# Kernel tuning notes

Hardware: AMD Instinct MI355X
Metric: run time of the kernel (lower is better)

Reference implementation:

```python
import jax, jax.numpy as jnp
import numpy as np

N_NODES = 50000
N_EDGES = 800000
D = 128
L = 3


def setup_inputs() -> dict:
    key = jax.random.key(0)
    k1, k2, k3 = jax.random.split(key, 3)
    x = jax.random.normal(k1, (N_NODES, D), dtype=jnp.float32)
    edge_index = jax.random.randint(k2, (2, N_EDGES), 0, N_NODES, dtype=jnp.int64)
    # per-layer GCNConv weights [L, in, out], bias [L, out] (zeros, as nn.Linear default bias is small),
    # PReLU per-channel slopes initialized to 0.25 (torch default)
    Ws = jax.random.normal(k3, (L, D, D), dtype=jnp.float32) / np.sqrt(D)
    bs = jnp.zeros((L, D), dtype=jnp.float32)
    alphas = jnp.full((L, D), 0.25, dtype=jnp.float32)
    return {"x": x, "edge_index": edge_index, "Ws": Ws, "bs": bs, "alphas": alphas}


def reference(x, edge_index, Ws, bs, alphas):
    N = x.shape[0]
    # PyG gcn_norm with edge_weight=None: unit weights, add self-loops (fill value 1),
    # symmetric normalization deg^{-1/2}[row] * deg^{-1/2}[col], aggregate at col (target).
    loop = jnp.arange(N, dtype=edge_index.dtype)
    row = jnp.concatenate([edge_index[0], loop])  # [E+N] source
    col = jnp.concatenate([edge_index[1], loop])  # [E+N] target
    deg = jax.ops.segment_sum(jnp.ones(row.shape[0], x.dtype), col, num_segments=N)
    dinv = jax.lax.rsqrt(deg)  # deg >= 1 due to self-loops
    norm = dinv[row] * dinv[col]  # [E+N]

    z = x
    for l in range(Ws.shape[0]):
        h = z @ Ws[l]  # linear transform [N, D]
        # gather -> scale -> scatter-add aggregation
        agg = jax.ops.segment_sum(h[row] * norm[:, None], col, num_segments=N)
        out = agg + bs[l]
        z = jnp.where(out >= 0, out, alphas[l] * out)  # per-channel PReLU
    return z
```

## Files before the change

### kernel.cpp

```cpp
#include <hip/hip_runtime.h>

#define N_NODES 50000
#define N_EDGES 800000
#define D 128
#define L 3
#define SCAN_B 1024
#define SCAN_NB ((N_NODES + SCAN_B - 1) / SCAN_B)


__global__ __launch_bounds__(256) void deg_init_k(unsigned int* deg) {
  int i = blockIdx.x * 256 + threadIdx.x;
  if (i < N_NODES) deg[i] = 1u;
}

__global__ __launch_bounds__(256) void deg_count_k(const int* __restrict__ col,
                                                   unsigned int* deg,
                                                   unsigned int* __restrict__ rank) {
  int e = blockIdx.x * 256 + threadIdx.x;
  if (e < N_EDGES) rank[e] = atomicAdd(&deg[col[e]], 1u);
}

__global__ __launch_bounds__(256) void dinv_k(float* dinv_f, const unsigned int* deg) {
  int i = blockIdx.x * 256 + threadIdx.x;
  if (i < N_NODES) dinv_f[i] = rsqrtf((float)deg[i]);
}

__global__ __launch_bounds__(SCAN_B) void scan1_k(const unsigned int* __restrict__ deg,
                                                  unsigned int* __restrict__ rowptr,
                                                  unsigned int* __restrict__ bsum) {
  __shared__ unsigned int buf[SCAN_B];
  const int tid = threadIdx.x;
  const int i = blockIdx.x * SCAN_B + tid;
  unsigned int d = (i < N_NODES) ? (deg[i] - 1u) : 0u;
  buf[tid] = d;
  __syncthreads();
  for (int off = 1; off < SCAN_B; off <<= 1) {
    unsigned int t = (tid >= off) ? buf[tid - off] : 0u;
    __syncthreads();
    buf[tid] += t;
    __syncthreads();
  }
  if (i < N_NODES) rowptr[i] = buf[tid] - d;
  if (tid == SCAN_B - 1) bsum[blockIdx.x] = buf[tid];
}

__global__ __launch_bounds__(64) void scan2_k(const unsigned int* __restrict__ bsum,
                                              unsigned int* __restrict__ boff,
                                              unsigned int* __restrict__ rowptr) {
  int lane = threadIdx.x;
  unsigned int v = (lane < SCAN_NB) ? bsum[lane] : 0u;
  unsigned int incl = v;
#pragma unroll
  for (int off = 1; off < 64; off <<= 1) {
    unsigned int t = __shfl_up(incl, off, 64);
    if (lane >= off) incl += t;
  }
  if (lane < SCAN_NB) boff[lane] = incl - v;
  if (lane == 63) rowptr[N_NODES] = incl;
}

__global__ __launch_bounds__(SCAN_B) void scan3_k(const unsigned int* __restrict__ boff,
                                                  unsigned int* __restrict__ rowptr) {
  int i = blockIdx.x * SCAN_B + threadIdx.x;
  if (i < N_NODES) rowptr[i] += boff[blockIdx.x];
}

__global__ __launch_bounds__(256) void fill_k(const int* __restrict__ rows,
                                              const int* __restrict__ cols,
                                              const unsigned int* __restrict__ rowptr,
                                              const unsigned int* __restrict__ rank,
                                              unsigned int* __restrict__ csr) {
  int e = blockIdx.x * 256 + threadIdx.x;
  if (e >= N_EDGES) return;
  csr[rowptr[cols[e]] + rank[e] - 1u] = (unsigned int)rows[e];
}

__global__ __launch_bounds__(256) void gather_k(const unsigned int* __restrict__ rowptr,
                                                const unsigned int* __restrict__ csr,
                                                const float* __restrict__ dinv,
                                                const float* __restrict__ Z,
                                                float* __restrict__ AGG) {
  int wid = (blockIdx.x * 256 + threadIdx.x) >> 6;
  int lane = threadIdx.x & 63;
  if (wid >= N_NODES) return;
  const float2* Z2 = (const float2*)Z;
  float di = dinv[wid];
  float2 z = Z2[(size_t)wid * 64 + lane];
  float sx = di * z.x, sy = di * z.y;
  unsigned int p = rowptr[wid], p1 = rowptr[wid + 1];
  for (; p + 4 <= p1; p += 4) {
    unsigned int s0 = csr[p], s1 = csr[p + 1], s2 = csr[p + 2], s3 = csr[p + 3];
    float w0 = dinv[s0], w1 = dinv[s1], w2 = dinv[s2], w3 = dinv[s3];
    float2 v0 = Z2[(size_t)s0 * 64 + lane];
    float2 v1 = Z2[(size_t)s1 * 64 + lane];
    float2 v2 = Z2[(size_t)s2 * 64 + lane];
    float2 v3 = Z2[(size_t)s3 * 64 + lane];
    sx += w0 * v0.x + w1 * v1.x + w2 * v2.x + w3 * v3.x;
    sy += w0 * v0.y + w1 * v1.y + w2 * v2.y + w3 * v3.y;
  }
  for (; p < p1; ++p) {
    unsigned int s0 = csr[p];
    float w0 = dinv[s0];
    float2 v0 = Z2[(size_t)s0 * 64 + lane];
    sx += w0 * v0.x;
    sy += w0 * v0.y;
  }
  float2 r;
  r.x = sx * di;
  r.y = sy * di;
  ((float2*)AGG)[(size_t)wid * 64 + lane] = r;
}

__global__ __launch_bounds__(256) void gemm_k(const float* __restrict__ P,
                                              const float* __restrict__ W,
                                              const float* __restrict__ bias,
                                              const float* __restrict__ alpha,
                                              float* __restrict__ out) {
  __shared__ float sW[32 * 128];
  __shared__ float sZ[128 * 33];
  const int tid = threadIdx.x;
  const int rb = blockIdx.x * 128;
  const int rg = tid >> 4, cg = tid & 15;
  const int r0 = rg * 8, c0 = cg * 8;
  float acc[8][8];
#pragma unroll
  for (int i = 0; i < 8; ++i)
#pragma unroll
    for (int j = 0; j < 8; ++j) acc[i][j] = 0.f;

  for (int kc = 0; kc < 128; kc += 32) {
    const float4* Wg = (const float4*)(W + (size_t)kc * 128);
#pragma unroll
    for (int i = 0; i < 4; ++i)
      ((float4*)sW)[tid + i * 256] = Wg[tid + i * 256];
#pragma unroll
    for (int i = 0; i < 4; ++i) {
      int idx = tid + i * 256;
      int r = idx >> 3, k4 = idx & 7;
      int gr = rb + r;
      float4 v = make_float4(0.f, 0.f, 0.f, 0.f);
      if (gr < N_NODES) v = *(const float4*)(P + (size_t)gr * D + kc + k4 * 4);
      float* dst = &sZ[r * 33 + k4 * 4];
      dst[0] = v.x; dst[1] = v.y; dst[2] = v.z; dst[3] = v.w;
    }
    __syncthreads();
#pragma unroll 8
    for (int k = 0; k < 32; ++k) {
      float zz[8], ww[8];
#pragma unroll
      for (int i = 0; i < 8; ++i) zz[i] = sZ[(r0 + i) * 33 + k];
      float4 wa = *(const float4*)&sW[k * 128 + c0];
      float4 wb = *(const float4*)&sW[k * 128 + c0 + 4];
      ww[0] = wa.x; ww[1] = wa.y; ww[2] = wa.z; ww[3] = wa.w;
      ww[4] = wb.x; ww[5] = wb.y; ww[6] = wb.z; ww[7] = wb.w;
#pragma unroll
      for (int i = 0; i < 8; ++i)
#pragma unroll
        for (int j = 0; j < 8; ++j) acc[i][j] = fmaf(zz[i], ww[j], acc[i][j]);
    }
    __syncthreads();
  }

  float bl[8], al[8];
#pragma unroll
  for (int j = 0; j < 8; ++j) {
    bl[j] = bias[c0 + j];
    al[j] = alpha[c0 + j];
  }
#pragma unroll
  for (int i = 0; i < 8; ++i) {
    int gr = rb + r0 + i;
    if (gr >= N_NODES) continue;
    float o[8];
#pragma unroll
    for (int j = 0; j < 8; ++j) {
      float v = acc[i][j] + bl[j];
      o[j] = v >= 0.f ? v : al[j] * v;
    }
    float4* dst = (float4*)(out + (size_t)gr * D + c0);
    dst[0] = make_float4(o[0], o[1], o[2], o[3]);
    dst[1] = make_float4(o[4], o[5], o[6], o[7]);
  }
}


extern "C" void kernel_launch(void* const* d_in, const int* in_sizes, int n_in,
                              void* d_out, int out_size, void* d_ws, size_t ws_size,
                              hipStream_t stream) {
  const float* x      = (const float*)d_in[0];
  const int*   ei     = (const int*)d_in[1];
  const float* Ws     = (const float*)d_in[2];
  const float* bs     = (const float*)d_in[3];
  const float* alphas = (const float*)d_in[4];
  float* out = (float*)d_out;

  const int* rows = ei;
  const int* cols = ei + N_EDGES;

  char* ws = (char*)d_ws;
  const size_t NPAD = (((size_t)N_NODES * 4 + 255) / 256) * 256;
  const size_t NP1PAD = ((((size_t)N_NODES + 1) * 4 + 255) / 256) * 256;
  float*        dinv   = (float*)ws;             ws += NPAD;
  unsigned int* rowptr = (unsigned int*)ws;      ws += NP1PAD;
  unsigned int* deg    = (unsigned int*)ws;      ws += NPAD;
  unsigned int* bsum   = (unsigned int*)ws;      ws += 256;
  unsigned int* boff   = (unsigned int*)ws;      ws += 256;
  unsigned int* csr    = (unsigned int*)ws;      ws += (size_t)N_EDGES * 4;
  float*        AGG    = (float*)ws;
  unsigned int* rank = (unsigned int*)AGG;
  float* Z = out;

  deg_init_k<<<(N_NODES + 255) / 256, 256, 0, stream>>>(deg);
  deg_count_k<<<(N_EDGES + 255) / 256, 256, 0, stream>>>(cols, deg, rank);
  dinv_k<<<(N_NODES + 255) / 256, 256, 0, stream>>>(dinv, deg);
  scan1_k<<<SCAN_NB, SCAN_B, 0, stream>>>(deg, rowptr, bsum);
  scan2_k<<<1, 64, 0, stream>>>(bsum, boff, rowptr);
  scan3_k<<<SCAN_NB, SCAN_B, 0, stream>>>(boff, rowptr);
  fill_k<<<(N_EDGES + 255) / 256, 256, 0, stream>>>(rows, cols, rowptr, rank, csr);

  for (int l = 0; l < L; ++l) {
    const float* zin = (l == 0) ? x : Z;
    gather_k<<<(N_NODES * 64 + 255) / 256, 256, 0, stream>>>(rowptr, csr, dinv, zin, AGG);
    gemm_k<<<(N_NODES + 127) / 128, 256, 0, stream>>>(
        AGG, Ws + (size_t)l * D * D, bs + (size_t)l * D, alphas + (size_t)l * D, Z);
  }
}
```

Baseline: 342.4 us.

## Cooperative wave-wide neighbor index loads in gather; transpose GEMM LDS tile for vector reads

In the aggregation kernel, each wave now loads up to 64 neighbor indices and their dinv weights in one coalesced read and broadcasts them with shuffles. It then issues 8 independent row loads at a time, replacing per-lane redundant scalar index and weight loads and raising memory-level parallelism. In the GEMM, the activation tile in shared memory is stored transposed with padding so the inner loop reads 8 rows with two float4 LDS loads instead of 8 scalar loads. The cost is strided scalar writes into LDS during tile fill and extra shuffle instructions in the gather.

Result: no change. 338.2 us (-1.2%).

```diff
diff --git a/kernel.cpp b/kernel.cpp
--- a/kernel.cpp
+++ b/kernel.cpp
@@ -87,23 +87,41 @@
   float di = dinv[wid];
   float2 z = Z2[(size_t)wid * 64 + lane];
   float sx = di * z.x, sy = di * z.y;
-  unsigned int p = rowptr[wid], p1 = rowptr[wid + 1];
-  for (; p + 4 <= p1; p += 4) {
-    unsigned int s0 = csr[p], s1 = csr[p + 1], s2 = csr[p + 2], s3 = csr[p + 3];
-    float w0 = dinv[s0], w1 = dinv[s1], w2 = dinv[s2], w3 = dinv[s3];
-    float2 v0 = Z2[(size_t)s0 * 64 + lane];
-    float2 v1 = Z2[(size_t)s1 * 64 + lane];
-    float2 v2 = Z2[(size_t)s2 * 64 + lane];
-    float2 v3 = Z2[(size_t)s3 * 64 + lane];
-    sx += w0 * v0.x + w1 * v1.x + w2 * v2.x + w3 * v3.x;
-    sy += w0 * v0.y + w1 * v1.y + w2 * v2.y + w3 * v3.y;
-  }
-  for (; p < p1; ++p) {
-    unsigned int s0 = csr[p];
-    float w0 = dinv[s0];
-    float2 v0 = Z2[(size_t)s0 * 64 + lane];
-    sx += w0 * v0.x;
-    sy += w0 * v0.y;
+  unsigned int p0 = rowptr[wid], p1 = rowptr[wid + 1];
+  for (unsigned int base = p0; base < p1; base += 64u) {
+    unsigned int cnt = p1 - base;
+    if (cnt > 64u) cnt = 64u;
+    unsigned int s = 0u;
+    float w = 0.f;
+    if (lane < (int)cnt) {
+      s = csr[base + lane];
+      w = dinv[s];
+    }
+    unsigned int j = 0;
+    for (; j + 8u <= cnt; j += 8u) {
+      unsigned int ss[8];
+      float wws[8];
+#pragma unroll
+      for (int t = 0; t < 8; ++t) {
+        ss[t] = __shfl(s, (int)(j + t), 64);
+        wws[t] = __shfl(w, (int)(j + t), 64);
+      }
+      float2 v[8];
+#pragma unroll
+      for (int t = 0; t < 8; ++t) v[t] = Z2[(size_t)ss[t] * 64 + lane];
+#pragma unroll
+      for (int t = 0; t < 8; ++t) {
+        sx += wws[t] * v[t].x;
+        sy += wws[t] * v[t].y;
+      }
+    }
+    for (; j < cnt; ++j) {
+      unsigned int s0 = __shfl(s, (int)j, 64);
+      float w0 = __shfl(w, (int)j, 64);
+      float2 v0 = Z2[(size_t)s0 * 64 + lane];
+      sx += w0 * v0.x;
+      sy += w0 * v0.y;
+    }
   }
   float2 r;
   r.x = sx * di;
@@ -117,7 +135,7 @@
                                               const float* __restrict__ alpha,
                                               float* __restrict__ out) {
   __shared__ float sW[32 * 128];
-  __shared__ float sZ[128 * 33];
+  __shared__ float sZT[32 * 132];
   const int tid = threadIdx.x;
   const int rb = blockIdx.x * 128;
   const int rg = tid >> 4, cg = tid & 15;
@@ -140,19 +158,20 @@
       int gr = rb + r;
       float4 v = make_float4(0.f, 0.f, 0.f, 0.f);
       if (gr < N_NODES) v = *(const float4*)(P + (size_t)gr * D + kc + k4 * 4);
-      float* dst = &sZ[r * 33 + k4 * 4];
-      dst[0] = v.x; dst[1] = v.y; dst[2] = v.z; dst[3] = v.w;
+      sZT[(k4 * 4 + 0) * 132 + r] = v.x;
+      sZT[(k4 * 4 + 1) * 132 + r] = v.y;
+      sZT[(k4 * 4 + 2) * 132 + r] = v.z;
+      sZT[(k4 * 4 + 3) * 132 + r] = v.w;
     }
     __syncthreads();
 #pragma unroll 8
     for (int k = 0; k < 32; ++k) {
-      float zz[8], ww[8];
-#pragma unroll
-      for (int i = 0; i < 8; ++i) zz[i] = sZ[(r0 + i) * 33 + k];
+      float4 za = *(const float4*)&sZT[k * 132 + r0];
+      float4 zb = *(const float4*)&sZT[k * 132 + r0 + 4];
       float4 wa = *(const float4*)&sW[k * 128 + c0];
       float4 wb = *(const float4*)&sW[k * 128 + c0 + 4];
-      ww[0] = wa.x; ww[1] = wa.y; ww[2] = wa.z; ww[3] = wa.w;
-      ww[4] = wb.x; ww[5] = wb.y; ww[6] = wb.z; ww[7] = wb.w;
+      float zz[8] = {za.x, za.y, za.z, za.w, zb.x, zb.y, zb.z, zb.w};
+      float ww[8] = {wa.x, wa.y, wa.z, wa.w, wb.x, wb.y, wb.z, wb.w};
 #pragma unroll
       for (int i = 0; i < 8; ++i)
 #pragma unroll
```
